# Performance work log

Hardware: AMD Instinct MI355X
Metric: run time of the kernel (lower is better)

## Reference

```python
import jax, jax.numpy as jnp
import numpy as np
from jax import lax


def _fuse_proj(proj):
    # proj: [B,2,4,4] -> [B,4,4]; K @ [R|t] into top 3x4 of extrinsics
    p = proj[:, 0]
    new34 = jnp.einsum('bij,bjk->bik', proj[:, 1, :3, :3], proj[:, 0, :3, :4])
    return p.at[:, :3, :4].set(new34)


def _homo_warp(src_fea, src_proj, ref_proj, depth_values):
    # src_fea [B,C,H,W], src_proj/ref_proj [B,4,4], depth_values [B,D]
    B, C, H, W = src_fea.shape
    D = depth_values.shape[1]
    proj = jnp.einsum('bij,bjk->bik', src_proj, jnp.linalg.inv(ref_proj))
    rot, trans = proj[:, :3, :3], proj[:, :3, 3:4]
    y, x = jnp.meshgrid(jnp.arange(H, dtype=src_fea.dtype),
                        jnp.arange(W, dtype=src_fea.dtype), indexing='ij')
    xyz = jnp.stack([x.ravel(), y.ravel(), jnp.ones(H * W, src_fea.dtype)])  # [3,HW]
    rot_xyz = jnp.einsum('bij,jk->bik', rot, xyz)                            # [B,3,HW]
    pxyz = rot_xyz[:, :, None, :] * depth_values[:, None, :, None] + trans[:, :, None, :]  # [B,3,D,HW]
    z = pxyz[:, 2]
    px = pxyz[:, 0] / z   # pixel coords (align_corners=True convention)
    py = pxyz[:, 1] / z
    # bilinear sample with zeros padding
    x0 = jnp.floor(px); y0 = jnp.floor(py)
    x1 = x0 + 1.0;      y1 = y0 + 1.0
    wx1 = px - x0; wx0 = 1.0 - wx1
    wy1 = py - y0; wy0 = 1.0 - wy1
    fea_flat = src_fea.reshape(B, C, H * W)

    def corner(xc, yc, w):
        valid = (xc >= 0) & (xc <= W - 1) & (yc >= 0) & (yc <= H - 1)
        idx = (jnp.clip(yc, 0, H - 1).astype(jnp.int32) * W
               + jnp.clip(xc, 0, W - 1).astype(jnp.int32)).reshape(B, -1)   # [B,D*HW]
        g = jax.vmap(lambda f, i: jnp.take(f, i, axis=1))(fea_flat, idx)    # [B,C,D*HW]
        return g * (w * valid.astype(w.dtype)).reshape(B, 1, -1)

    out = (corner(x0, y0, wx0 * wy0) + corner(x1, y0, wx1 * wy0)
           + corner(x0, y1, wx0 * wy1) + corner(x1, y1, wx1 * wy1))
    return out.reshape(B, C, D, H, W)


def _forward(features, proj_matrices, depth_values, reg_w, num_depth):
    N = features.shape[0]
    ref_fea = features[0]                      # [B,C,H,W]
    ref_proj = _fuse_proj(proj_matrices[:, 0])
    B, C, H, W = ref_fea.shape
    D = num_depth

    vol_sum = jnp.broadcast_to(ref_fea[:, :, None], (B, C, D, H, W))
    vol_sq = vol_sum ** 2
    for i in range(1, N):                      # small fixed view loop
        src_proj = _fuse_proj(proj_matrices[:, i])
        wv = _homo_warp(features[i], src_proj, ref_proj, depth_values)
        vol_sum = vol_sum + wv
        vol_sq = vol_sq + wv ** 2
    inv_n = 1.0 / N
    variance = vol_sq * inv_n - (vol_sum * inv_n) ** 2   # [B,C,D,H,W]

    # cost regularization: 3x3x3 conv C->1 (stand-in for external 3D CNN)
    cost = lax.conv_general_dilated(variance, reg_w, (1, 1, 1), 'SAME',
                                    dimension_numbers=('NCDHW', 'OIDHW', 'NCDHW'))[:, 0]  # [B,D,H,W]
    prob = jax.nn.softmax(cost, axis=1)
    depth = jnp.sum(prob * depth_values[:, :, None, None], axis=1)          # [B,H,W]

    # photometric confidence (no-grad block)
    p = lax.stop_gradient(prob)
    # 4*avg_pool3d(pad(prob,(1,2)) over depth, kernel (4,1,1)) == sliding sum of 4
    sum4 = lax.reduce_window(p, 0.0, lax.add, (1, 4, 1, 1), (1, 1, 1, 1),
                             ((0, 0), (1, 2), (0, 0), (0, 0)))
    didx = jnp.sum(p * jnp.arange(D, dtype=p.dtype)[None, :, None, None], axis=1)
    didx = jnp.clip(didx.astype(jnp.int32), 0, D - 1)                        # [B,H,W]
    conf = jnp.take_along_axis(sum4, didx[:, None], axis=1)[:, 0]            # [B,H,W]
    return depth, conf


def setup_inputs() -> dict:
    key = jax.random.key(0)
    k1, k2, k3 = jax.random.split(key, 3)
    N, B, C, H, W, D = 5, 1, 32, 128, 160, 48
    features = jax.random.normal(k1, (N, B, C, H, W), jnp.float32)
    eye = jnp.eye(4, dtype=jnp.float32)
    proj_matrices = eye + 0.01 * jax.random.normal(k2, (B, N, 2, 4, 4), jnp.float32)
    depth_values = jnp.broadcast_to(
        425.0 + 510.0 * jnp.arange(D, dtype=jnp.float32) / (D - 1), (B, D))
    reg_w = 0.05 * jax.random.normal(k3, (1, C, 3, 3, 3), jnp.float32)
    return {"features": features, "proj_matrices": proj_matrices,
            "depth_values": depth_values, "reg_w": reg_w, "num_depth": D}


def reference(features, proj_matrices, depth_values, reg_w, num_depth):
    return _forward(features, proj_matrices, depth_values, reg_w, num_depth)
```

## Files before the change

### kernel.cpp

```cpp
#include <hip/hip_runtime.h>

#define W_ 160
#define H_ 128
#define C_ 32
#define D_ 48
#define HW_ (H_*W_)
#define TX 16
#define TY 16
#define HPX 18
#define HPY 18
#define NHP (HPX*HPY)
#define NHPP 336
#define DST 28

typedef _Float16 h8 __attribute__((ext_vector_type(8)));
typedef __fp16 fp16x2 __attribute__((ext_vector_type(2)));
typedef float f4 __attribute__((ext_vector_type(4)));

__device__ __forceinline__ _Float16 u2h(unsigned int u) {
    union { unsigned short s; _Float16 h; } x; x.s = (unsigned short)u; return x.h;
}
__device__ __forceinline__ unsigned int pkh2(float a, float b) {
    union { fp16x2 h; unsigned int u; } x;
    x.h = __builtin_amdgcn_cvt_pkrtz(a, b);
    return x.u;
}

__device__ __forceinline__ void inv4x4(const float* a, float* inv) {
    inv[0]  =  a[5]*a[10]*a[15] - a[5]*a[11]*a[14] - a[9]*a[6]*a[15] + a[9]*a[7]*a[14] + a[13]*a[6]*a[11] - a[13]*a[7]*a[10];
    inv[4]  = -a[4]*a[10]*a[15] + a[4]*a[11]*a[14] + a[8]*a[6]*a[15] - a[8]*a[7]*a[14] - a[12]*a[6]*a[11] + a[12]*a[7]*a[10];
    inv[8]  =  a[4]*a[9]*a[15]  - a[4]*a[11]*a[13] - a[8]*a[5]*a[15] + a[8]*a[7]*a[13] + a[12]*a[5]*a[11] - a[12]*a[7]*a[9];
    inv[12] = -a[4]*a[9]*a[14]  + a[4]*a[10]*a[13] + a[8]*a[5]*a[14] - a[8]*a[6]*a[13] - a[12]*a[5]*a[10] + a[12]*a[6]*a[9];
    inv[1]  = -a[1]*a[10]*a[15] + a[1]*a[11]*a[14] + a[9]*a[2]*a[15] - a[9]*a[3]*a[14] - a[13]*a[2]*a[11] + a[13]*a[3]*a[10];
    inv[5]  =  a[0]*a[10]*a[15] - a[0]*a[11]*a[14] - a[8]*a[2]*a[15] + a[8]*a[3]*a[14] + a[12]*a[2]*a[11] - a[12]*a[3]*a[10];
    inv[9]  = -a[0]*a[9]*a[15]  + a[0]*a[11]*a[13] + a[8]*a[1]*a[15] - a[8]*a[3]*a[13] - a[12]*a[1]*a[11] + a[12]*a[3]*a[9];
    inv[13] =  a[0]*a[9]*a[14]  - a[0]*a[10]*a[13] - a[8]*a[1]*a[14] + a[8]*a[2]*a[13] + a[12]*a[1]*a[10] - a[12]*a[2]*a[9];
    inv[2]  =  a[1]*a[6]*a[15]  - a[1]*a[7]*a[14]  - a[5]*a[2]*a[15] + a[5]*a[3]*a[14] + a[13]*a[2]*a[7]  - a[13]*a[3]*a[6];
    inv[6]  = -a[0]*a[6]*a[15]  + a[0]*a[7]*a[14]  + a[4]*a[2]*a[15] - a[4]*a[3]*a[14] - a[12]*a[2]*a[7]  + a[12]*a[3]*a[6];
    inv[10] =  a[0]*a[5]*a[15]  - a[0]*a[7]*a[13]  - a[4]*a[1]*a[15] + a[4]*a[3]*a[13] + a[12]*a[1]*a[7]  - a[12]*a[3]*a[5];
    inv[14] = -a[0]*a[5]*a[14]  + a[0]*a[6]*a[13]  + a[4]*a[1]*a[14] - a[4]*a[2]*a[13] - a[12]*a[1]*a[6]  + a[12]*a[2]*a[5];
    inv[3]  = -a[1]*a[6]*a[11]  + a[1]*a[7]*a[10]  + a[5]*a[2]*a[11] - a[5]*a[3]*a[10] - a[9]*a[2]*a[7]   + a[9]*a[3]*a[6];
    inv[7]  =  a[0]*a[6]*a[11]  - a[0]*a[7]*a[10]  - a[4]*a[2]*a[11] + a[4]*a[3]*a[10] + a[8]*a[2]*a[7]   - a[8]*a[3]*a[6];
    inv[11] = -a[0]*a[5]*a[11]  + a[0]*a[7]*a[9]   + a[4]*a[1]*a[11] - a[4]*a[3]*a[9]  - a[8]*a[1]*a[7]   + a[8]*a[3]*a[5];
    inv[15] =  a[0]*a[5]*a[10]  - a[0]*a[6]*a[9]   - a[4]*a[1]*a[10] + a[4]*a[2]*a[9]  + a[8]*a[1]*a[6]   - a[8]*a[2]*a[5];
    float det = a[0]*inv[0] + a[1]*inv[4] + a[2]*inv[8] + a[3]*inv[12];
    float id = 1.0f / det;
    for (int i = 0; i < 16; ++i) inv[i] *= id;
}

__device__ __forceinline__ void fuseProj(const float* proj, int i, float* F) {
    const float* A = proj + i*32;
    const float* R = A + 16;
    for (int r = 0; r < 3; ++r)
        for (int k = 0; k < 4; ++k)
            F[r*4+k] = R[r*4]*A[k] + R[r*4+1]*A[4+k] + R[r*4+2]*A[8+k];
    for (int k = 0; k < 4; ++k) F[12+k] = A[12+k];
}

__global__ __launch_bounds__(256) void kS(const float* __restrict__ f,
                                          const float* __restrict__ proj,
                                          _Float16* __restrict__ ft,
                                          float* __restrict__ RX,
                                          float* __restrict__ M) {
    __shared__ float t[64][33];
    const int bx = blockIdx.x, v = blockIdx.y;
    const int tid = threadIdx.x;
    if (bx < 320) {
        const int p0 = bx * 64;
        const int pl = tid & 63;
        const int cb = (tid >> 6) * 8;
        #pragma unroll
        for (int k = 0; k < 8; ++k)
            t[pl][cb + k] = f[(size_t)(v*C_ + cb + k)*HW_ + p0 + pl];
        __syncthreads();
        const int px = tid >> 2;
        const int c0 = (tid & 3) * 8;
        h8 o;
        #pragma unroll
        for (int k = 0; k < 8; ++k) o[k] = (_Float16)t[px][c0 + k];
        *(h8*)&ft[((size_t)(v*HW_ + p0 + px) << 5) + c0] = o;
    } else {
        if (v >= 4) return;
        float F0[16], Fv[16], inv[16], P[12];
        fuseProj(proj, 0, F0);
        fuseProj(proj, v + 1, Fv);
        inv4x4(F0, inv);
        #pragma unroll
        for (int r = 0; r < 3; ++r)
            #pragma unroll
            for (int c = 0; c < 4; ++c) {
                float acc = 0.f;
                #pragma unroll
                for (int k = 0; k < 4; ++k) acc += Fv[r*4+k]*inv[k*4+c];
                P[r*4+c] = acc;
            }
        const int p = (bx - 320)*256 + tid;
        const float x = (float)(p % W_), y = (float)(p / W_);
        float4 o;
        o.x = P[0]*x + P[1]*y + P[2];
        o.y = P[4]*x + P[5]*y + P[6];
        o.z = P[8]*x + P[9]*y + P[10];
        o.w = 0.f;
        ((float4*)RX)[(size_t)v*HW_ + p] = o;
        if (bx == 320 && tid == 0) {
            float* om = M + v*12;
            om[0]=P[0]; om[1]=P[1]; om[2]=P[2];
            om[3]=P[4]; om[4]=P[5]; om[5]=P[6];
            om[6]=P[8]; om[7]=P[9]; om[8]=P[10];
            om[9]=P[3]; om[10]=P[7]; om[11]=P[11];
        }
    }
}

__global__ __launch_bounds__(256) void kA(const _Float16* __restrict__ featH,
                                          const float* __restrict__ RX,
                                          const float* __restrict__ M,
                                          const float* __restrict__ dvals,
                                          const float* __restrict__ regw,
                                          float* __restrict__ Q) {
    __shared__ __align__(16) _Float16 VT[NHPP*32];
    __shared__ __align__(16) unsigned int SMA[4704];
    __shared__ float Tsh[12];
    unsigned int* PI  = SMA;
    unsigned int* PWA = SMA + 4*NHP;
    unsigned int* PWB = SMA + 8*NHP;
    _Float16* DL = (_Float16*)SMA;

    const int tid = threadIdx.x;
    const int bx = blockIdx.x, by = blockIdx.y, d = blockIdx.z;
    const int lane = tid & 63;
    const float dv = dvals[d];

    if (tid < 12) Tsh[tid] = M[(tid/3)*12 + 9 + (tid % 3)];

    h8 bf0, bf1;
    {
        const int n = lane & 15;
        const int kb = (lane >> 4) * 8;
        #pragma unroll
        for (int j = 0; j < 8; ++j) {
            const int ch = kb + j;
            bf0[j] = (_Float16)regw[ch*27 + n];
            bf1[j] = (_Float16)((n < 11) ? regw[ch*27 + 16 + n] : 0.f);
        }
    }
    __syncthreads();

    #pragma unroll 1
    for (int pp = 0; pp < 2; ++pp) {
        const int px = pp*256 + tid;
        if (px >= NHP) continue;
        const int hx = px % HPX;
        const int hy = px / HPX;
        const int lx = bx*TX + hx - 1;
        const int ly = by*TY + hy - 1;
        if (lx < 0 || lx >= W_ || ly < 0 || ly >= H_) {
            #pragma unroll
            for (int v = 0; v < 4; ++v) {
                PI[v*NHP+px] = 0u; PWA[v*NHP+px] = 0u; PWB[v*NHP+px] = 0u;
            }
        } else {
            const int rp = ly*W_ + lx;
            #pragma unroll
            for (int v = 0; v < 4; ++v) {
                const float4 a = ((const float4*)RX)[(size_t)v*HW_ + rp];
                const float z  = a.z*dv + Tsh[v*3+2];
                const float rz = 1.0f / z;
                const float pxf = (a.x*dv + Tsh[v*3+0])*rz;
                const float pyf = (a.y*dv + Tsh[v*3+1])*rz;
                const float x0f = floorf(pxf), y0f = floorf(pyf);
                const float wx1 = pxf - x0f, wy1 = pyf - y0f;
                const float vx0 = (x0f >= 0.f && x0f <= (float)(W_-1)) ? 1.f : 0.f;
                const float vx1 = (x0f >= -1.f && x0f <= (float)(W_-2)) ? 1.f : 0.f;
                const float vy0 = (y0f >= 0.f && y0f <= (float)(H_-1)) ? 1.f : 0.f;
                const float vy1 = (y0f >= -1.f && y0f <= (float)(H_-2)) ? 1.f : 0.f;
                const int ix0 = (int)fminf(fmaxf(x0f,      0.f), (float)(W_-1));
                const int ix1 = (int)fminf(fmaxf(x0f + 1.f,0.f), (float)(W_-1));
                const int iy0 = (int)fminf(fmaxf(y0f,      0.f), (float)(H_-1));
                const int iy1 = (int)fminf(fmaxf(y0f + 1.f,0.f), (float)(H_-1));
                const float wx0v = (1.f - wx1)*vx0, wx1v = wx1*vx1;
                const float wy0v = (1.f - wy1)*vy0, wy1v = wy1*vy1;
                PI [v*NHP+px] = (unsigned)ix0 | ((unsigned)ix1 << 8)
                              | ((unsigned)iy0 << 16) | ((unsigned)iy1 << 24);
                PWA[v*NHP+px] = pkh2(wx0v*wy0v, wx1v*wy0v);
                PWB[v*NHP+px] = pkh2(wx0v*wy1v, wx1v*wy1v);
            }
        }
    }
    __syncthreads();

    const h8 hz = {(_Float16)0,(_Float16)0,(_Float16)0,(_Float16)0,
                   (_Float16)0,(_Float16)0,(_Float16)0,(_Float16)0};
    const h8* F = (const h8*)featH;
    #pragma unroll 1
    for (int pass = 0; pass < 6; ++pass) {
        const int idx = pass*256 + tid;
        if (idx >= NHPP*4) continue;
        const int px = idx >> 2, u = idx & 3;
        h8 var = hz;
        if (px < NHP) {
            const int hx = px % HPX;
            const int hy = px / HPX;
            const int lx = bx*TX + hx - 1;
            const int ly = by*TY + hy - 1;
            h8 s = hz, q = hz;
            if (lx >= 0 && lx < W_ && ly >= 0 && ly < H_) {
                const h8 f = F[(size_t)(ly*W_ + lx)*4 + u];
                s = f; q = f*f;
            }
            #pragma unroll
            for (int v = 0; v < 4; ++v) {
                const unsigned ri = PI [v*NHP+px];
                const unsigned wa = PWA[v*NHP+px];
                const unsigned wb = PWB[v*NHP+px];
                const int x0 = ri & 0xff, x1 = (ri >> 8) & 0xff;
                const int y0W = ((ri >> 16) & 0xff) * W_;
                const int y1W = (ri >> 24) * W_;
                const h8* Fv = F + (size_t)(v+1)*HW_*4;
                const h8 f00 = Fv[(y0W+x0)*4 + u];
                const h8 f10 = Fv[(y0W+x1)*4 + u];
                const h8 f01 = Fv[(y1W+x0)*4 + u];
                const h8 f11 = Fv[(y1W+x1)*4 + u];
                const _Float16 w00 = u2h(wa), w10 = u2h(wa >> 16);
                const _Float16 w01 = u2h(wb), w11 = u2h(wb >> 16);
                const h8 g = f00*w00 + f10*w10 + f01*w01 + f11*w11;
                s += g;
                q += g*g;
            }
            const _Float16 c5 = (_Float16)0.2f;
            const h8 s5 = s * c5;
            var = q * c5 - s5*s5;
        }
        *(h8*)&VT[px*32 + u*8] = var;
    }
    __syncthreads();

    {
        const int wv = tid >> 6;
        const int n = lane & 15;
        const int grp = lane >> 4;
        const f4 fz = {0.f, 0.f, 0.f, 0.f};
        #pragma unroll 1
        for (int tile = wv; tile < NHPP/16; tile += 4) {
            const h8 a = *(const h8*)&VT[(tile*16 + n)*32 + grp*8];
            const f4 d0 = __builtin_amdgcn_mfma_f32_16x16x32_f16(a, bf0, fz, 0, 0, 0);
            const f4 d1 = __builtin_amdgcn_mfma_f32_16x16x32_f16(a, bf1, fz, 0, 0, 0);
            const int rbase = tile*16 + grp*4;
            #pragma unroll
            for (int r = 0; r < 4; ++r) {
                _Float16* dr = &DL[(rbase + r)*DST];
                dr[n] = (_Float16)d0[r];
                if (n < 11) dr[16 + n] = (_Float16)d1[r];
            }
        }
    }
    __syncthreads();

    {
        const int x = tid & 15;
        const int y = tid >> 4;
        float c0 = 0.f, c1 = 0.f, c2 = 0.f;
        #pragma unroll
        for (int jy = 0; jy < 3; ++jy) {
            #pragma unroll
            for (int jx = 0; jx < 3; ++jx) {
                const int hp = (y + jy)*HPX + (x + jx);
                const int sp = jy*3 + jx;
                const _Float16* dr = &DL[hp*DST];
                c0 += (float)dr[sp];
                c1 += (float)dr[9 + sp];
                c2 += (float)dr[18 + sp];
            }
        }
        const int p = (by*TY + y)*W_ + bx*TX + x;
        Q[(size_t)(0*D_ + d)*HW_ + p] = c0;
        Q[(size_t)(1*D_ + d)*HW_ + p] = c1;
        Q[(size_t)(2*D_ + d)*HW_ + p] = c2;
    }
}

__global__ __launch_bounds__(128) void kB(const float* __restrict__ Q,
                                          const float* __restrict__ dvals,
                                          float* __restrict__ out) {
    const int p = blockIdx.x*128 + threadIdx.x;
    const float* Q0 = Q;
    const float* Q1 = Q + (size_t)D_*HW_;
    const float* Q2 = Q + (size_t)2*D_*HW_;
    float pr[D_];
    #pragma unroll
    for (int d = 0; d < D_; ++d) {
        float c = Q1[d*HW_ + p];
        if (d > 0)     c += Q0[(d-1)*HW_ + p];
        if (d < D_-1)  c += Q2[(d+1)*HW_ + p];
        pr[d] = c;
    }
    float m = pr[0];
    #pragma unroll
    for (int d = 1; d < D_; ++d) m = fmaxf(m, pr[d]);
    float s = 0.f;
    #pragma unroll
    for (int d = 0; d < D_; ++d) { const float e = __expf(pr[d] - m); pr[d] = e; s += e; }
    const float is = 1.f / s;
    float depth = 0.f, fidx = 0.f;
    #pragma unroll
    for (int d = 0; d < D_; ++d) {
        const float pp = pr[d] * is;
        pr[d] = pp;
        depth += pp * dvals[d];
        fidx  += pp * (float)d;
    }
    int di = (int)fidx;
    di = di < 0 ? 0 : (di > D_-1 ? D_-1 : di);
    float conf = 0.f;
    #pragma unroll
    for (int d = 0; d < D_; ++d)
        conf += ((d >= di-1) && (d <= di+2)) ? pr[d] : 0.f;
    out[p] = depth;
    out[HW_ + p] = conf;
}

extern "C" void kernel_launch(void* const* d_in, const int* in_sizes, int n_in,
                              void* d_out, int out_size, void* d_ws, size_t ws_size,
                              hipStream_t stream) {
    const float* features = (const float*)d_in[0];
    const float* proj     = (const float*)d_in[1];
    const float* dvals    = (const float*)d_in[2];
    const float* regw     = (const float*)d_in[3];
    float* out = (float*)d_out;

    _Float16* featH = (_Float16*)d_ws;
    float* RX = (float*)(featH + (size_t)5*HW_*C_);
    float* M  = RX + (size_t)4*HW_*4;
    float* Q  = M + 64;

    kS<<<dim3(400, 5), 256, 0, stream>>>(features, proj, featH, RX, M);
    kA<<<dim3(W_/TX, H_/TY, D_), 256, 0, stream>>>(featH, RX, M, dvals, regw, Q);
    kB<<<HW_/128, 128, 0, stream>>>(Q, dvals, out);
}
```

Before: 154.7 us.

## Process two depth planes per block and fuse warp sampling into MFMA tiles

Each kA block now handles two adjacent depth planes. It computes the warp coordinates inline rather than staging indices and weights in shared memory, and each wave feeds its computed variance straight into the MFMA without the VT staging buffer. The reference-feature load and RX fetch are shared across both depths, and the four corner gathers are reused when the second depth lands on the same integer cell. This is meant to cut shared-memory traffic and barriers and to halve the redundant per-pixel loads. In exchange, per-thread register pressure goes up, there is a divergent reload branch, and the grid has half as many blocks.

```diff
diff --git a/kernel.cpp b/kernel.cpp
--- a/kernel.cpp
+++ b/kernel.cpp
@@ -11,20 +11,11 @@
 #define HPY 18
 #define NHP (HPX*HPY)
 #define NHPP 336
+#define NT 21
 #define DST 28
 
 typedef _Float16 h8 __attribute__((ext_vector_type(8)));
-typedef __fp16 fp16x2 __attribute__((ext_vector_type(2)));
 typedef float f4 __attribute__((ext_vector_type(4)));
-
-__device__ __forceinline__ _Float16 u2h(unsigned int u) {
-    union { unsigned short s; _Float16 h; } x; x.s = (unsigned short)u; return x.h;
-}
-__device__ __forceinline__ unsigned int pkh2(float a, float b) {
-    union { fp16x2 h; unsigned int u; } x;
-    x.h = __builtin_amdgcn_cvt_pkrtz(a, b);
-    return x.u;
-}
 
 __device__ __forceinline__ void inv4x4(const float* a, float* inv) {
     inv[0]  =  a[5]*a[10]*a[15] - a[5]*a[11]*a[14] - a[9]*a[6]*a[15] + a[9]*a[7]*a[14] + a[13]*a[6]*a[11] - a[13]*a[7]*a[10];
@@ -112,31 +103,27 @@
     }
 }
 
-__global__ __launch_bounds__(256) void kA(const _Float16* __restrict__ featH,
-                                          const float* __restrict__ RX,
-                                          const float* __restrict__ M,
-                                          const float* __restrict__ dvals,
-                                          const float* __restrict__ regw,
-                                          float* __restrict__ Q) {
-    __shared__ __align__(16) _Float16 VT[NHPP*32];
-    __shared__ __align__(16) unsigned int SMA[4704];
-    __shared__ float Tsh[12];
-    unsigned int* PI  = SMA;
-    unsigned int* PWA = SMA + 4*NHP;
-    unsigned int* PWB = SMA + 8*NHP;
-    _Float16* DL = (_Float16*)SMA;
+__global__ __launch_bounds__(256, 4) void kA(const _Float16* __restrict__ featH,
+                                             const float* __restrict__ RX,
+                                             const float* __restrict__ M,
+                                             const float* __restrict__ dvals,
+                                             const float* __restrict__ regw,
+                                             float* __restrict__ Q) {
+    __shared__ __align__(16) _Float16 DL0[NHPP*DST];
+    __shared__ __align__(16) _Float16 DL1[NHPP*DST];
 
     const int tid = threadIdx.x;
-    const int bx = blockIdx.x, by = blockIdx.y, d = blockIdx.z;
+    const int bx = blockIdx.x, by = blockIdx.y;
+    const int d0 = blockIdx.z*2, d1 = d0 + 1;
     const int lane = tid & 63;
-    const float dv = dvals[d];
-
-    if (tid < 12) Tsh[tid] = M[(tid/3)*12 + 9 + (tid % 3)];
+    const int wv = tid >> 6;
+    const int n = lane & 15;
+    const int grp = lane >> 4;
+    const float dv0 = dvals[d0], dv1 = dvals[d1];
 
     h8 bf0, bf1;
     {
-        const int n = lane & 15;
-        const int kb = (lane >> 4) * 8;
+        const int kb = grp * 8;
         #pragma unroll
         for (int j = 0; j < 8; ++j) {
             const int ch = kb + j;
@@ -144,113 +131,103 @@
             bf1[j] = (_Float16)((n < 11) ? regw[ch*27 + 16 + n] : 0.f);
         }
     }
-    __syncthreads();
+
+    const h8 hz = {(_Float16)0,(_Float16)0,(_Float16)0,(_Float16)0,
+                   (_Float16)0,(_Float16)0,(_Float16)0,(_Float16)0};
+    const h8* F = (const h8*)featH;
+    const float4* RX4 = (const float4*)RX;
+    const f4 fz = {0.f, 0.f, 0.f, 0.f};
 
     #pragma unroll 1
-    for (int pp = 0; pp < 2; ++pp) {
-        const int px = pp*256 + tid;
-        if (px >= NHP) continue;
+    for (int pass = 0; pass < 6; ++pass) {
+        const int tile = pass*4 + wv;
+        if (tile >= NT) continue;
+        const int px = tile*16 + n;
+        h8 var0 = hz, var1 = hz;
         const int hx = px % HPX;
         const int hy = px / HPX;
         const int lx = bx*TX + hx - 1;
         const int ly = by*TY + hy - 1;
-        if (lx < 0 || lx >= W_ || ly < 0 || ly >= H_) {
+        if (px < NHP && lx >= 0 && lx < W_ && ly >= 0 && ly < H_) {
+            const int rp = ly*W_ + lx;
+            const h8 fr = F[(size_t)rp*4 + grp];
+            h8 s0 = fr, q0 = fr*fr, s1 = fr, q1 = fr*fr;
             #pragma unroll
             for (int v = 0; v < 4; ++v) {
-                PI[v*NHP+px] = 0u; PWA[v*NHP+px] = 0u; PWB[v*NHP+px] = 0u;
-            }
-        } else {
-            const int rp = ly*W_ + lx;
-            #pragma unroll
-            for (int v = 0; v < 4; ++v) {
-                const float4 a = ((const float4*)RX)[(size_t)v*HW_ + rp];
-                const float z  = a.z*dv + Tsh[v*3+2];
-                const float rz = 1.0f / z;
-                const float pxf = (a.x*dv + Tsh[v*3+0])*rz;
-                const float pyf = (a.y*dv + Tsh[v*3+1])*rz;
-                const float x0f = floorf(pxf), y0f = floorf(pyf);
-                const float wx1 = pxf - x0f, wy1 = pyf - y0f;
-                const float vx0 = (x0f >= 0.f && x0f <= (float)(W_-1)) ? 1.f : 0.f;
-                const float vx1 = (x0f >= -1.f && x0f <= (float)(W_-2)) ? 1.f : 0.f;
-                const float vy0 = (y0f >= 0.f && y0f <= (float)(H_-1)) ? 1.f : 0.f;
-                const float vy1 = (y0f >= -1.f && y0f <= (float)(H_-2)) ? 1.f : 0.f;
-                const int ix0 = (int)fminf(fmaxf(x0f,      0.f), (float)(W_-1));
-                const int ix1 = (int)fminf(fmaxf(x0f + 1.f,0.f), (float)(W_-1));
-                const int iy0 = (int)fminf(fmaxf(y0f,      0.f), (float)(H_-1));
-                const int iy1 = (int)fminf(fmaxf(y0f + 1.f,0.f), (float)(H_-1));
-                const float wx0v = (1.f - wx1)*vx0, wx1v = wx1*vx1;
-                const float wy0v = (1.f - wy1)*vy0, wy1v = wy1*vy1;
-                PI [v*NHP+px] = (unsigned)ix0 | ((unsigned)ix1 << 8)
-                              | ((unsigned)iy0 << 16) | ((unsigned)iy1 << 24);
-                PWA[v*NHP+px] = pkh2(wx0v*wy0v, wx1v*wy0v);
-                PWB[v*NHP+px] = pkh2(wx0v*wy1v, wx1v*wy1v);
-            }
-        }
-    }
-    __syncthreads();
-
-    const h8 hz = {(_Float16)0,(_Float16)0,(_Float16)0,(_Float16)0,
-                   (_Float16)0,(_Float16)0,(_Float16)0,(_Float16)0};
-    const h8* F = (const h8*)featH;
-    #pragma unroll 1
-    for (int pass = 0; pass < 6; ++pass) {
-        const int idx = pass*256 + tid;
-        if (idx >= NHPP*4) continue;
-        const int px = idx >> 2, u = idx & 3;
-        h8 var = hz;
-        if (px < NHP) {
-            const int hx = px % HPX;
-            const int hy = px / HPX;
-            const int lx = bx*TX + hx - 1;
-            const int ly = by*TY + hy - 1;
-            h8 s = hz, q = hz;
-            if (lx >= 0 && lx < W_ && ly >= 0 && ly < H_) {
-                const h8 f = F[(size_t)(ly*W_ + lx)*4 + u];
-                s = f; q = f*f;
-            }
-            #pragma unroll
-            for (int v = 0; v < 4; ++v) {
-                const unsigned ri = PI [v*NHP+px];
-                const unsigned wa = PWA[v*NHP+px];
-                const unsigned wb = PWB[v*NHP+px];
-                const int x0 = ri & 0xff, x1 = (ri >> 8) & 0xff;
-                const int y0W = ((ri >> 16) & 0xff) * W_;
-                const int y1W = (ri >> 24) * W_;
+                const float4 a = RX4[(size_t)v*HW_ + rp];
+                const float tx = M[v*12+9], ty = M[v*12+10], tz = M[v*12+11];
+                const float z0 = a.z*dv0 + tz;
+                const float rz0 = 1.0f / z0;
+                const float pxf0 = (a.x*dv0 + tx)*rz0;
+                const float pyf0 = (a.y*dv0 + ty)*rz0;
+                const float fx0 = floorf(pxf0), fy0 = floorf(pyf0);
+                const float wxf0 = pxf0 - fx0, wyf0 = pyf0 - fy0;
+                const float vxl0 = (fx0 >= 0.f  && fx0 <= 159.f) ? 1.f : 0.f;
+                const float vxh0 = (fx0 >= -1.f && fx0 <= 158.f) ? 1.f : 0.f;
+                const float vyl0 = (fy0 >= 0.f  && fy0 <= 127.f) ? 1.f : 0.f;
+                const float vyh0 = (fy0 >= -1.f && fy0 <= 126.f) ? 1.f : 0.f;
+                const int xs0 = (int)fminf(fmaxf(fx0 + 1.f, 0.f), 160.f);
+                const int ys0 = (int)fminf(fmaxf(fy0 + 1.f, 0.f), 128.f);
+                const int x0 = max(xs0-1, 0), x1 = min(xs0, W_-1);
+                const int y0W = max(ys0-1, 0)*W_, y1W = min(ys0, H_-1)*W_;
+                const _Float16 w00a = (_Float16)((1.f-wxf0)*vxl0 * (1.f-wyf0)*vyl0);
+                const _Float16 w10a = (_Float16)(wxf0*vxh0 * (1.f-wyf0)*vyl0);
+                const _Float16 w01a = (_Float16)((1.f-wxf0)*vxl0 * wyf0*vyh0);
+                const _Float16 w11a = (_Float16)(wxf0*vxh0 * wyf0*vyh0);
                 const h8* Fv = F + (size_t)(v+1)*HW_*4;
-                const h8 f00 = Fv[(y0W+x0)*4 + u];
-                const h8 f10 = Fv[(y0W+x1)*4 + u];
-                const h8 f01 = Fv[(y1W+x0)*4 + u];
-                const h8 f11 = Fv[(y1W+x1)*4 + u];
-                const _Float16 w00 = u2h(wa), w10 = u2h(wa >> 16);
-                const _Float16 w01 = u2h(wb), w11 = u2h(wb >> 16);
-                const h8 g = f00*w00 + f10*w10 + f01*w01 + f11*w11;
-                s += g;
-                q += g*g;
+                const h8 f00 = Fv[(size_t)(y0W+x0)*4 + grp];
+                const h8 f10 = Fv[(size_t)(y0W+x1)*4 + grp];
+                const h8 f01 = Fv[(size_t)(y1W+x0)*4 + grp];
+                const h8 f11 = Fv[(size_t)(y1W+x1)*4 + grp];
+                const h8 g0 = f00*w00a + f10*w10a + f01*w01a + f11*w11a;
+                s0 += g0; q0 += g0*g0;
+                const float z1 = a.z*dv1 + tz;
+                const float rz1 = 1.0f / z1;
+                const float pxf1 = (a.x*dv1 + tx)*rz1;
+                const float pyf1 = (a.y*dv1 + ty)*rz1;
+                const float fx1 = floorf(pxf1), fy1 = floorf(pyf1);
+                const float wxf1 = pxf1 - fx1, wyf1 = pyf1 - fy1;
+                const float vxl1 = (fx1 >= 0.f  && fx1 <= 159.f) ? 1.f : 0.f;
+                const float vxh1 = (fx1 >= -1.f && fx1 <= 158.f) ? 1.f : 0.f;
+                const float vyl1 = (fy1 >= 0.f  && fy1 <= 127.f) ? 1.f : 0.f;
+                const float vyh1 = (fy1 >= -1.f && fy1 <= 126.f) ? 1.f : 0.f;
+                const int xs1 = (int)fminf(fmaxf(fx1 + 1.f, 0.f), 160.f);
+                const int ys1 = (int)fminf(fmaxf(fy1 + 1.f, 0.f), 128.f);
+                const _Float16 w00b = (_Float16)((1.f-wxf1)*vxl1 * (1.f-wyf1)*vyl1);
+                const _Float16 w10b = (_Float16)(wxf1*vxh1 * (1.f-wyf1)*vyl1);
+                const _Float16 w01b = (_Float16)((1.f-wxf1)*vxl1 * wyf1*vyh1);
+                const _Float16 w11b = (_Float16)(wxf1*vxh1 * wyf1*vyh1);
+                h8 F00 = f00, F10 = f10, F01 = f01, F11 = f11;
+                if ((xs1 != xs0) || (ys1 != ys0)) {
+                    const int xa = max(xs1-1, 0), xb = min(xs1, W_-1);
+                    const int yaW = max(ys1-1, 0)*W_, ybW = min(ys1, H_-1)*W_;
+                    F00 = Fv[(size_t)(yaW+xa)*4 + grp];
+                    F10 = Fv[(size_t)(yaW+xb)*4 + grp];
+                    F01 = Fv[(size_t)(ybW+xa)*4 + grp];
+                    F11 = Fv[(size_t)(ybW+xb)*4 + grp];
+                }
+                const h8 g1 = F00*w00b + F10*w10b + F01*w01b + F11*w11b;
+                s1 += g1; q1 += g1*g1;
             }
             const _Float16 c5 = (_Float16)0.2f;
-            const h8 s5 = s * c5;
-            var = q * c5 - s5*s5;
-        }
-        *(h8*)&VT[px*32 + u*8] = var;
-    }
-    __syncthreads();
-
-    {
-        const int wv = tid >> 6;
-        const int n = lane & 15;
-        const int grp = lane >> 4;
-        const f4 fz = {0.f, 0.f, 0.f, 0.f};
-        #pragma unroll 1
-        for (int tile = wv; tile < NHPP/16; tile += 4) {
-            const h8 a = *(const h8*)&VT[(tile*16 + n)*32 + grp*8];
-            const f4 d0 = __builtin_amdgcn_mfma_f32_16x16x32_f16(a, bf0, fz, 0, 0, 0);
-            const f4 d1 = __builtin_amdgcn_mfma_f32_16x16x32_f16(a, bf1, fz, 0, 0, 0);
-            const int rbase = tile*16 + grp*4;
-            #pragma unroll
-            for (int r = 0; r < 4; ++r) {
-                _Float16* dr = &DL[(rbase + r)*DST];
-                dr[n] = (_Float16)d0[r];
-                if (n < 11) dr[16 + n] = (_Float16)d1[r];
+            const h8 sa = s0 * c5, sb = s1 * c5;
+            var0 = q0*c5 - sa*sa;
+            var1 = q1*c5 - sb*sb;
+        }
+        const f4 a0 = __builtin_amdgcn_mfma_f32_16x16x32_f16(var0, bf0, fz, 0, 0, 0);
+        const f4 b0 = __builtin_amdgcn_mfma_f32_16x16x32_f16(var0, bf1, fz, 0, 0, 0);
+        const f4 a1 = __builtin_amdgcn_mfma_f32_16x16x32_f16(var1, bf0, fz, 0, 0, 0);
+        const f4 b1 = __builtin_amdgcn_mfma_f32_16x16x32_f16(var1, bf1, fz, 0, 0, 0);
+        const int rbase = tile*16 + grp*4;
+        #pragma unroll
+        for (int r = 0; r < 4; ++r) {
+            _Float16* dr0 = &DL0[(rbase + r)*DST];
+            _Float16* dr1 = &DL1[(rbase + r)*DST];
+            dr0[n] = (_Float16)a0[r];
+            dr1[n] = (_Float16)a1[r];
+            if (n < 11) {
+                dr0[16 + n] = (_Float16)b0[r];
+                dr1[16 + n] = (_Float16)b1[r];
             }
         }
     }
@@ -259,23 +236,31 @@
     {
         const int x = tid & 15;
         const int y = tid >> 4;
-        float c0 = 0.f, c1 = 0.f, c2 = 0.f;
+        float c00 = 0.f, c01 = 0.f, c02 = 0.f;
+        float c10 = 0.f, c11 = 0.f, c12 = 0.f;
         #pragma unroll
         for (int jy = 0; jy < 3; ++jy) {
             #pragma unroll
             for (int jx = 0; jx < 3; ++jx) {
                 const int hp = (y + jy)*HPX + (x + jx);
                 const int sp = jy*3 + jx;
-                const _Float16* dr = &DL[hp*DST];
-                c0 += (float)dr[sp];
-                c1 += (float)dr[9 + sp];
-                c2 += (float)dr[18 + sp];
+                const _Float16* dr0 = &DL0[hp*DST];
+                const _Float16* dr1 = &DL1[hp*DST];
+                c00 += (float)dr0[sp];
+                c01 += (float)dr0[9 + sp];
+                c02 += (float)dr0[18 + sp];
+                c10 += (float)dr1[sp];
+                c11 += (float)dr1[9 + sp];
+                c12 += (float)dr1[18 + sp];
             }
         }
         const int p = (by*TY + y)*W_ + bx*TX + x;
-        Q[(size_t)(0*D_ + d)*HW_ + p] = c0;
-        Q[(size_t)(1*D_ + d)*HW_ + p] = c1;
-        Q[(size_t)(2*D_ + d)*HW_ + p] = c2;
+        Q[(size_t)(0*D_ + d0)*HW_ + p] = c00;
+        Q[(size_t)(1*D_ + d0)*HW_ + p] = c01;
+        Q[(size_t)(2*D_ + d0)*HW_ + p] = c02;
+        Q[(size_t)(0*D_ + d1)*HW_ + p] = c10;
+        Q[(size_t)(1*D_ + d1)*HW_ + p] = c11;
+        Q[(size_t)(2*D_ + d1)*HW_ + p] = c12;
     }
 }
 
@@ -334,6 +319,6 @@
     float* Q  = M + 64;
 
     kS<<<dim3(400, 5), 256, 0, stream>>>(features, proj, featH, RX, M);
-    kA<<<dim3(W_/TX, H_/TY, D_), 256, 0, stream>>>(featH, RX, M, dvals, regw, Q);
+    kA<<<dim3(W_/TX, H_/TY, D_/2), 256, 0, stream>>>(featH, RX, M, dvals, regw, Q);
     kB<<<HW_/128, 128, 0, stream>>>(Q, dvals, out);
 }
```

Result: slower. 344.2 us (+122.6%).
